# Performance work log

Measured on AMD Instinct MI355X. Metric: run time of the kernel, lower is better.

The kernel has to match this reference:

```python
import jax, jax.numpy as jnp
import numpy as np

N_NODES = 100000
N_EDGES = 1600000
NFEAT, NHID, NCLASS = 256, 256, 64
NLAYERS = 4


def _gcn_norm(edge_index, n_nodes):
    # PyG GCNConv default: add self-loops, symmetric normalization
    src, dst = edge_index[0], edge_index[1]
    loop = jnp.arange(n_nodes, dtype=edge_index.dtype)
    src = jnp.concatenate([src, loop])
    dst = jnp.concatenate([dst, loop])
    deg = jax.ops.segment_sum(jnp.ones_like(dst, dtype=jnp.float32), dst,
                              num_segments=n_nodes)
    dinv = jnp.where(deg > 0, jax.lax.rsqrt(deg), 0.0)
    norm = dinv[src] * dinv[dst]  # [E+N]
    return src, dst, norm


def _gcn_layer(X, W, b, src, dst, norm, n_nodes):
    H = X @ W                      # [N, out]
    msg = H[src] * norm[:, None]   # [E+N, out] gather + scale
    out = jax.ops.segment_sum(msg, dst, num_segments=n_nodes)
    return out + b


def setup_inputs() -> dict:
    key = jax.random.key(0)
    ks = jax.random.split(key, 8)
    x = jax.random.normal(ks[0], (N_NODES, NFEAT), dtype=jnp.float32)
    edge_index = jax.random.randint(ks[1], (2, N_EDGES), 0, N_NODES, dtype=jnp.int32)
    def glorot(k, fan_in, fan_out):
        s = jnp.sqrt(6.0 / (fan_in + fan_out))
        return jax.random.uniform(k, (fan_in, fan_out), jnp.float32, -s, s)
    return {
        "x": x,
        "W_enc": glorot(ks[2], NFEAT, NHID),
        "b_enc": jnp.zeros((NHID,), jnp.float32),
        "W_conv": glorot(ks[3], NHID, NHID),
        "b_conv": jnp.zeros((NHID,), jnp.float32),
        "W_dec": glorot(ks[4], NHID, NCLASS),
        "b_dec": jnp.zeros((NCLASS,), jnp.float32),
        "edge_index": edge_index,
    }


def reference(x, W_enc, b_enc, W_conv, b_conv, W_dec, b_dec, edge_index):
    n_nodes = x.shape[0]
    src, dst, norm = _gcn_norm(edge_index, n_nodes)
    # dropout probs are 0 (drop_in=drop=0) -> identity
    X = jax.nn.relu(_gcn_layer(x, W_enc, b_enc, src, dst, norm, n_nodes))
    for _ in range(NLAYERS):
        X = jax.nn.relu(_gcn_layer(X, W_conv, b_conv, src, dst, norm, n_nodes))
    X = jax.nn.relu(_gcn_layer(X, W_dec, b_dec, src, dst, norm, n_nodes))
    return X
```

## Files before the change

### kernel.cpp

```cpp
#include <hip/hip_runtime.h>

#define N_NODES 100000
#define N_EDGES 1600000
#define MPAD    100096
#define NB_SCAN ((N_NODES + 255) / 256)

using short8  = __attribute__((ext_vector_type(8))) short;
using ushort8 = __attribute__((ext_vector_type(8))) unsigned short;
using f32x4   = __attribute__((ext_vector_type(4))) float;

__device__ inline unsigned short f2bf(float f) {
    unsigned u = __float_as_uint(f);
    unsigned r = (u + 0x7fffu + ((u >> 16) & 1u)) >> 16;
    return (unsigned short)r;
}
__device__ inline float bf2f(unsigned short h) {
    return __uint_as_float(((unsigned)h) << 16);
}


__global__ __launch_bounds__(256) void k_init(int* __restrict__ indeg, int n) {
    int i = blockIdx.x * blockDim.x + threadIdx.x;
    if (i < n) indeg[i] = 0;
}

__global__ __launch_bounds__(256) void k_indeg(const int* __restrict__ dst,
                                               int* __restrict__ indeg, int e) {
    int i = (blockIdx.x * blockDim.x + threadIdx.x) * 4;
    if (i < e) {
        int4 d = *(const int4*)(dst + i);
        atomicAdd(&indeg[d.x], 1);
        atomicAdd(&indeg[d.y], 1);
        atomicAdd(&indeg[d.z], 1);
        atomicAdd(&indeg[d.w], 1);
    }
}

__global__ __launch_bounds__(256) void k_scan_blocks(const int* __restrict__ indeg,
                                                     int* __restrict__ blksum, int n) {
    int i = blockIdx.x * 256 + threadIdx.x;
    int v = (i < n) ? indeg[i] : 0;
#pragma unroll
    for (int o = 32; o > 0; o >>= 1) v += __shfl_down(v, o, 64);
    __shared__ int ws[4];
    if ((threadIdx.x & 63) == 0) ws[threadIdx.x >> 6] = v;
    __syncthreads();
    if (threadIdx.x == 0) blksum[blockIdx.x] = ws[0] + ws[1] + ws[2] + ws[3];
}

__global__ __launch_bounds__(512) void k_scan_top(const int* __restrict__ blksum,
                                                  int* __restrict__ blkpref,
                                                  int* __restrict__ offsets, int nb, int n) {
    __shared__ int s[512];
    int t = threadIdx.x;
    int v = (t < nb) ? blksum[t] : 0;
    s[t] = v;
    __syncthreads();
    for (int o = 1; o < 512; o <<= 1) {
        int u = (t >= o) ? s[t - o] : 0;
        __syncthreads();
        s[t] += u;
        __syncthreads();
    }
    if (t < nb) blkpref[t] = (t == 0) ? 0 : s[t - 1];
    if (t == nb - 1) offsets[n] = s[t];
}

__global__ __launch_bounds__(256) void k_scan_final(const int* __restrict__ indeg,
                                                    const int* __restrict__ blkpref,
                                                    int* __restrict__ offsets,
                                                    float* __restrict__ dinv, int n) {
    __shared__ int s[256];
    int t = threadIdx.x;
    int i = blockIdx.x * 256 + t;
    int v = (i < n) ? indeg[i] : 0;
    s[t] = v;
    __syncthreads();
    for (int o = 1; o < 256; o <<= 1) {
        int u = (t >= o) ? s[t - o] : 0;
        __syncthreads();
        s[t] += u;
        __syncthreads();
    }
    if (i < n) {
        offsets[i] = blkpref[blockIdx.x] + s[t] - v;
        dinv[i] = rsqrtf((float)(v + 1));
    }
}

__global__ __launch_bounds__(256) void k_scatter(const int* __restrict__ src,
                                                 const int* __restrict__ dst,
                                                 const int* __restrict__ offsets,
                                                 int* __restrict__ indeg,
                                                 int* __restrict__ csr_src, int e) {
    int i = blockIdx.x * blockDim.x + threadIdx.x;
    if (i < e) {
        int d = dst[i];
        int pos = offsets[d] + atomicSub(&indeg[d], 1) - 1;
        csr_src[pos] = src[i];
    }
}


__global__ __launch_bounds__(256) void k_cvt_x(const float* __restrict__ x,
                                               unsigned short* __restrict__ xb) {
    int i = blockIdx.x * blockDim.x + threadIdx.x;
    int row = i >> 6;
    ushort4 o;
    if (row < N_NODES) {
        float4 v = *(const float4*)(x + (size_t)i * 4);
        o.x = f2bf(v.x); o.y = f2bf(v.y); o.z = f2bf(v.z); o.w = f2bf(v.w);
    } else {
        o.x = o.y = o.z = o.w = 0;
    }
    *(ushort4*)(xb + (size_t)i * 4) = o;
}

__global__ __launch_bounds__(256) void k_prep_w(const float* __restrict__ W,
                                                unsigned short* __restrict__ Wt, int N) {
    int i = blockIdx.x * blockDim.x + threadIdx.x;
    if (i < 256 * N) {
        int r = i / N, c = i - r * N;
        Wt[(size_t)c * 256 + r] = f2bf(W[i]);
    }
}


template <int BN>
__global__ __launch_bounds__(256) void k_mfma_gemm(const unsigned short* __restrict__ A,
                                                   const unsigned short* __restrict__ Bt,
                                                   const float* __restrict__ dinv,
                                                   unsigned short* __restrict__ C,
                                                   int Ntot) {
    constexpr int K = 256, BK = 64;
    constexpr int NFR = BN / 32;
    __shared__ char ldsA[128 * 128];
    __shared__ char ldsB[BN * 128];
    const int tid  = threadIdx.x;
    const int lane = tid & 63;
    const int wid  = tid >> 6;
    const int wr   = wid >> 1, wc = wid & 1;
    const int row0 = blockIdx.x * 128;
    const int col0 = blockIdx.y * BN;
    const int l15  = lane & 15, lhi = lane >> 4;

    f32x4 acc[4][NFR];
#pragma unroll
    for (int m = 0; m < 4; ++m)
#pragma unroll
        for (int n = 0; n < NFR; ++n) acc[m][n] = {0.f, 0.f, 0.f, 0.f};

    for (int k0 = 0; k0 < K; k0 += BK) {
#pragma unroll
        for (int j = 0; j < 4; ++j) {
            int ci = j * 256 + tid;
            int r = ci >> 3;
            int cb = (ci & 7) ^ (r & 7);
            const char* src = (const char*)(A + (size_t)(row0 + r) * K + k0) + cb * 16;
            __builtin_amdgcn_global_load_lds((const __attribute__((address_space(1))) void*)src,
                                             (__attribute__((address_space(3))) void*)(ldsA + ci * 16),
                                             16, 0, 0);
        }
#pragma unroll
        for (int j = 0; j < BN / 32; ++j) {
            int ci = j * 256 + tid;
            int r = ci >> 3;
            int cb = (ci & 7) ^ (r & 7);
            const char* src = (const char*)(Bt + (size_t)(col0 + r) * K + k0) + cb * 16;
            __builtin_amdgcn_global_load_lds((const __attribute__((address_space(1))) void*)src,
                                             (__attribute__((address_space(3))) void*)(ldsB + ci * 16),
                                             16, 0, 0);
        }
        __syncthreads();
#pragma unroll
        for (int kk = 0; kk < 2; ++kk) {
            short8 af[4], bfr[NFR];
            int cb = kk * 4 + lhi;
#pragma unroll
            for (int m = 0; m < 4; ++m) {
                int r = wr * 64 + m * 16 + l15;
                af[m] = *(const short8*)(ldsA + r * 128 + ((cb ^ (r & 7)) << 4));
            }
#pragma unroll
            for (int n = 0; n < NFR; ++n) {
                int r = wc * (NFR * 16) + n * 16 + l15;
                bfr[n] = *(const short8*)(ldsB + r * 128 + ((cb ^ (r & 7)) << 4));
            }
#pragma unroll
            for (int m = 0; m < 4; ++m)
#pragma unroll
                for (int n = 0; n < NFR; ++n)
                    acc[m][n] = __builtin_amdgcn_mfma_f32_16x16x32_bf16(af[m], bfr[n],
                                                                        acc[m][n], 0, 0, 0);
        }
        __syncthreads();
    }
#pragma unroll
    for (int m = 0; m < 4; ++m) {
        int rbase = row0 + wr * 64 + m * 16 + lhi * 4;
        float sc[4];
#pragma unroll
        for (int q = 0; q < 4; ++q) {
            int grow = rbase + q;
            sc[q] = (grow < N_NODES) ? dinv[grow] : 0.f;
        }
#pragma unroll
        for (int n = 0; n < NFR; ++n) {
            int col = col0 + wc * (NFR * 16) + n * 16 + l15;
#pragma unroll
            for (int q = 0; q < 4; ++q)
                C[(size_t)(rbase + q) * Ntot + col] = f2bf(acc[m][n][q] * sc[q]);
        }
    }
}


__global__ __launch_bounds__(256) void k_agg256(const unsigned short* __restrict__ H,
                                                const int* __restrict__ offsets,
                                                const int* __restrict__ csr_src,
                                                const float* __restrict__ dinv,
                                                const float* __restrict__ bias,
                                                unsigned short* __restrict__ out, int n) {
    const int w = __builtin_amdgcn_readfirstlane((blockIdx.x * blockDim.x + threadIdx.x) >> 6);
    const int n0 = w * 2;
    if (n0 >= n) return;
    const int n1 = n0 + 1;
    const int lane = threadIdx.x & 63;
    const int half = lane >> 5;
    const unsigned coff = (unsigned)(lane & 31) * 16u;

    float a0[8] = {}, a1[8] = {};
    int e0 = offsets[n0];
    const int f0 = offsets[n1];
    int e1 = f0;
    const int f1 = offsets[n1 + 1];

    auto pair0 = [&](int ea) {
        int s0 = csr_src[ea], s1 = csr_src[ea + 1];
        ushort8 v = *(const ushort8*)((const char*)H + (unsigned)(half ? s1 : s0) * 512u + coff);
#pragma unroll
        for (int j = 0; j < 8; ++j) a0[j] += bf2f(v[j]);
    };
    auto pair1 = [&](int ea) {
        int s0 = csr_src[ea], s1 = csr_src[ea + 1];
        ushort8 v = *(const ushort8*)((const char*)H + (unsigned)(half ? s1 : s0) * 512u + coff);
#pragma unroll
        for (int j = 0; j < 8; ++j) a1[j] += bf2f(v[j]);
    };

    while (e0 + 3 < f0 && e1 + 3 < f1) {
        pair0(e0); pair0(e0 + 2);
        pair1(e1); pair1(e1 + 2);
        e0 += 4; e1 += 4;
    }
    while (e0 + 1 < f0 && e1 + 1 < f1) { pair0(e0); pair1(e1); e0 += 2; e1 += 2; }
    while (e0 + 1 < f0) { pair0(e0); e0 += 2; }
    while (e1 + 1 < f1) { pair1(e1); e1 += 2; }

    {
        int has = (e0 < f0);
        int sA = has ? csr_src[e0] : n0;
        float wB = has ? 1.f : 0.f;
        unsigned off = (unsigned)(half ? n0 : sA) * 512u + coff;
        float wgt = half ? wB : 1.f;
        ushort8 v = *(const ushort8*)((const char*)H + off);
#pragma unroll
        for (int j = 0; j < 8; ++j) a0[j] = fmaf(bf2f(v[j]), wgt, a0[j]);
    }
    {
        int has = (e1 < f1);
        int sA = has ? csr_src[e1] : n1;
        float wB = has ? 1.f : 0.f;
        unsigned off = (unsigned)(half ? n1 : sA) * 512u + coff;
        float wgt = half ? wB : 1.f;
        ushort8 v = *(const ushort8*)((const char*)H + off);
#pragma unroll
        for (int j = 0; j < 8; ++j) a1[j] = fmaf(bf2f(v[j]), wgt, a1[j]);
    }

#pragma unroll
    for (int j = 0; j < 8; ++j) {
        a0[j] += __shfl_xor(a0[j], 32);
        a1[j] += __shfl_xor(a1[j], 32);
    }

    if (half == 0) {
        const float* bp = bias + (lane & 31) * 8;
        float4 b0 = *(const float4*)bp;
        float4 b1 = *(const float4*)(bp + 4);
        float d0 = dinv[n0], d1 = dinv[n1];
        ushort8 o0, o1;
        o0[0] = f2bf(fmaxf(fmaf(a0[0], d0, b0.x), 0.f));
        o0[1] = f2bf(fmaxf(fmaf(a0[1], d0, b0.y), 0.f));
        o0[2] = f2bf(fmaxf(fmaf(a0[2], d0, b0.z), 0.f));
        o0[3] = f2bf(fmaxf(fmaf(a0[3], d0, b0.w), 0.f));
        o0[4] = f2bf(fmaxf(fmaf(a0[4], d0, b1.x), 0.f));
        o0[5] = f2bf(fmaxf(fmaf(a0[5], d0, b1.y), 0.f));
        o0[6] = f2bf(fmaxf(fmaf(a0[6], d0, b1.z), 0.f));
        o0[7] = f2bf(fmaxf(fmaf(a0[7], d0, b1.w), 0.f));
        o1[0] = f2bf(fmaxf(fmaf(a1[0], d1, b0.x), 0.f));
        o1[1] = f2bf(fmaxf(fmaf(a1[1], d1, b0.y), 0.f));
        o1[2] = f2bf(fmaxf(fmaf(a1[2], d1, b0.z), 0.f));
        o1[3] = f2bf(fmaxf(fmaf(a1[3], d1, b0.w), 0.f));
        o1[4] = f2bf(fmaxf(fmaf(a1[4], d1, b1.x), 0.f));
        o1[5] = f2bf(fmaxf(fmaf(a1[5], d1, b1.y), 0.f));
        o1[6] = f2bf(fmaxf(fmaf(a1[6], d1, b1.z), 0.f));
        o1[7] = f2bf(fmaxf(fmaf(a1[7], d1, b1.w), 0.f));
        *(ushort8*)((char*)out + (unsigned)n0 * 512u + coff) = o0;
        *(ushort8*)((char*)out + (unsigned)n1 * 512u + coff) = o1;
    }
}


__global__ __launch_bounds__(256) void k_agg64(const unsigned short* __restrict__ H,
                                               const int* __restrict__ offsets,
                                               const int* __restrict__ csr_src,
                                               const float* __restrict__ dinv,
                                               const float* __restrict__ bias,
                                               float* __restrict__ out, int n) {
    const int wid = __builtin_amdgcn_readfirstlane((blockIdx.x * blockDim.x + threadIdx.x) >> 6);
    if (wid >= n) return;
    const int lane = threadIdx.x & 63;
    const int q = lane >> 4;
    const unsigned coff = (unsigned)(lane & 15) * 8u;

    float acc[4] = {};
    const int beg = offsets[wid], end = offsets[wid + 1];
    int e = beg;

    for (; e + 3 < end; e += 4) {
        int s0 = csr_src[e], s1 = csr_src[e + 1], s2 = csr_src[e + 2], s3 = csr_src[e + 3];
        int srow = s0;
        if (q == 1) srow = s1;
        else if (q == 2) srow = s2;
        else if (q == 3) srow = s3;
        ushort4 v = *(const ushort4*)((const char*)H + (unsigned)srow * 128u + coff);
        acc[0] += bf2f(v.x); acc[1] += bf2f(v.y);
        acc[2] += bf2f(v.z); acc[3] += bf2f(v.w);
    }
    {
        int r = end - e;
        int srow = wid; float wgt = 0.f;
        if (q < r) { srow = csr_src[e + q]; wgt = 1.f; }
        else if (q == r) { srow = wid; wgt = 1.f; }
        ushort4 v = *(const ushort4*)((const char*)H + (unsigned)srow * 128u + coff);
        acc[0] = fmaf(bf2f(v.x), wgt, acc[0]);
        acc[1] = fmaf(bf2f(v.y), wgt, acc[1]);
        acc[2] = fmaf(bf2f(v.z), wgt, acc[2]);
        acc[3] = fmaf(bf2f(v.w), wgt, acc[3]);
    }
#pragma unroll
    for (int j = 0; j < 4; ++j) {
        acc[j] += __shfl_xor(acc[j], 16);
        acc[j] += __shfl_xor(acc[j], 32);
    }
    if (q == 0) {
        float dv = dinv[wid];
        float4 b = *(const float4*)(bias + (lane & 15) * 4);
        float4 o = make_float4(fmaxf(fmaf(acc[0], dv, b.x), 0.f),
                               fmaxf(fmaf(acc[1], dv, b.y), 0.f),
                               fmaxf(fmaf(acc[2], dv, b.z), 0.f),
                               fmaxf(fmaf(acc[3], dv, b.w), 0.f));
        *(float4*)((char*)out + (size_t)wid * 256u + coff * 2u) = o;
    }
}


extern "C" void kernel_launch(void* const* d_in, const int* in_sizes, int n_in,
                              void* d_out, int out_size, void* d_ws, size_t ws_size,
                              hipStream_t stream) {
    const float* x      = (const float*)d_in[0];
    const float* W_enc  = (const float*)d_in[1];
    const float* b_enc  = (const float*)d_in[2];
    const float* W_conv = (const float*)d_in[3];
    const float* b_conv = (const float*)d_in[4];
    const float* W_dec  = (const float*)d_in[5];
    const float* b_dec  = (const float*)d_in[6];
    const int*   ei     = (const int*)d_in[7];

    const int N = N_NODES;
    const int E = N_EDGES;
    const int* src = ei;
    const int* dst = ei + E;

    size_t off = 0;
    auto carve = [&](size_t bytes) -> void* {
        void* p = (char*)d_ws + off;
        off = (off + bytes + 255) & ~(size_t)255;
        return p;
    };
    unsigned short* Xb      = (unsigned short*)carve((size_t)MPAD * 256 * 2);
    unsigned short* Hb      = (unsigned short*)carve((size_t)MPAD * 256 * 2);
    unsigned short* Wt_enc  = (unsigned short*)carve((size_t)256 * 256 * 2);
    unsigned short* Wt_conv = (unsigned short*)carve((size_t)256 * 256 * 2);
    unsigned short* Wt_dec  = (unsigned short*)carve((size_t)64 * 256 * 2);
    int*            indeg   = (int*)carve((size_t)N * sizeof(int));
    float*          dinv    = (float*)carve((size_t)N * sizeof(float));
    int*            offsets = (int*)carve((size_t)(N + 1) * sizeof(int));
    int*            csr_src = (int*)carve((size_t)E * sizeof(int));
    int*            blksum  = (int*)carve((size_t)NB_SCAN * sizeof(int));
    int*            blkpref = (int*)carve((size_t)NB_SCAN * sizeof(int));
    (void)ws_size;

    k_cvt_x<<<MPAD / 4, 256, 0, stream>>>(x, Xb);
    k_prep_w<<<(256 * 256 + 255) / 256, 256, 0, stream>>>(W_enc, Wt_enc, 256);
    k_prep_w<<<(256 * 256 + 255) / 256, 256, 0, stream>>>(W_conv, Wt_conv, 256);
    k_prep_w<<<(256 * 64 + 255) / 256, 256, 0, stream>>>(W_dec, Wt_dec, 64);
    k_init<<<(N + 255) / 256, 256, 0, stream>>>(indeg, N);
    k_indeg<<<(E / 4 + 255) / 256, 256, 0, stream>>>(dst, indeg, E);
    k_scan_blocks<<<NB_SCAN, 256, 0, stream>>>(indeg, blksum, N);
    k_scan_top<<<1, 512, 0, stream>>>(blksum, blkpref, offsets, NB_SCAN, N);
    k_scan_final<<<NB_SCAN, 256, 0, stream>>>(indeg, blkpref, offsets, dinv, N);
    k_scatter<<<(E + 255) / 256, 256, 0, stream>>>(src, dst, offsets, indeg, csr_src, E);

    dim3 gconv(MPAD / 128, 2);
    dim3 gdec(MPAD / 128, 1);
    const int agg2_blocks = ((N + 1) / 2 + 3) / 4;
    const int agg1_blocks = (N + 3) / 4;

    k_mfma_gemm<128><<<gconv, 256, 0, stream>>>(Xb, Wt_enc, dinv, Hb, 256);
    k_agg256<<<agg2_blocks, 256, 0, stream>>>(Hb, offsets, csr_src, dinv, b_enc, Xb, N);
    for (int l = 0; l < 4; ++l) {
        k_mfma_gemm<128><<<gconv, 256, 0, stream>>>(Xb, Wt_conv, dinv, Hb, 256);
        k_agg256<<<agg2_blocks, 256, 0, stream>>>(Hb, offsets, csr_src, dinv, b_conv, Xb, N);
    }
    k_mfma_gemm<64><<<gdec, 256, 0, stream>>>(Xb, Wt_dec, dinv, Hb, 64);
    k_agg64<<<agg1_blocks, 256, 0, stream>>>(Hb, offsets, csr_src, dinv, b_dec,
                                             (float*)d_out, N);
}
```

Measured before the change: 1.041 ms.

## Fuse aggregation and GEMM for conv layers using aggregate-then-transform ordering

The four hidden conv layers now run one fused kernel instead of a GEMM plus an aggregation kernel. Each block first aggregates 64 destination rows of pre-scaled features into LDS, then multiplies by W with MFMA and applies bias, ReLU and dinv in the epilogue. The previous layer's output is pre-multiplied by dinv, so the decoder GEMM drops its own dinv scaling. This removes the intermediate H round trip through HBM and half the launches. The costs are that W is read straight from global memory per block, the gather phase may run at lower occupancy because of the 32KB LDS tile, and extra bf16 rounding now happens after the aggregation step.

```diff
diff --git a/kernel.cpp b/kernel.cpp
--- a/kernel.cpp
+++ b/kernel.cpp
@@ -126,7 +126,7 @@
 }
 
 
-template <int BN>
+template <int BN, bool DSCALE>
 __global__ __launch_bounds__(256) void k_mfma_gemm(const unsigned short* __restrict__ A,
                                                    const unsigned short* __restrict__ Bt,
                                                    const float* __restrict__ dinv,
@@ -202,7 +202,7 @@
 #pragma unroll
         for (int q = 0; q < 4; ++q) {
             int grow = rbase + q;
-            sc[q] = (grow < N_NODES) ? dinv[grow] : 0.f;
+            sc[q] = DSCALE ? ((grow < N_NODES) ? dinv[grow] : 0.f) : 1.f;
         }
 #pragma unroll
         for (int n = 0; n < NFR; ++n) {
@@ -261,9 +261,8 @@
         int has = (e0 < f0);
         int sA = has ? csr_src[e0] : n0;
         float wB = has ? 1.f : 0.f;
-        unsigned off = (unsigned)(half ? n0 : sA) * 512u + coff;
+        ushort8 v = *(const ushort8*)((const char*)H + (unsigned)(half ? n0 : sA) * 512u + coff);
         float wgt = half ? wB : 1.f;
-        ushort8 v = *(const ushort8*)((const char*)H + off);
 #pragma unroll
         for (int j = 0; j < 8; ++j) a0[j] = fmaf(bf2f(v[j]), wgt, a0[j]);
     }
@@ -271,9 +270,8 @@
         int has = (e1 < f1);
         int sA = has ? csr_src[e1] : n1;
         float wB = has ? 1.f : 0.f;
-        unsigned off = (unsigned)(half ? n1 : sA) * 512u + coff;
+        ushort8 v = *(const ushort8*)((const char*)H + (unsigned)(half ? n1 : sA) * 512u + coff);
         float wgt = half ? wB : 1.f;
-        ushort8 v = *(const ushort8*)((const char*)H + off);
 #pragma unroll
         for (int j = 0; j < 8; ++j) a1[j] = fmaf(bf2f(v[j]), wgt, a1[j]);
     }
@@ -289,25 +287,122 @@
         float4 b0 = *(const float4*)bp;
         float4 b1 = *(const float4*)(bp + 4);
         float d0 = dinv[n0], d1 = dinv[n1];
+        float bb[8] = {b0.x, b0.y, b0.z, b0.w, b1.x, b1.y, b1.z, b1.w};
         ushort8 o0, o1;
-        o0[0] = f2bf(fmaxf(fmaf(a0[0], d0, b0.x), 0.f));
-        o0[1] = f2bf(fmaxf(fmaf(a0[1], d0, b0.y), 0.f));
-        o0[2] = f2bf(fmaxf(fmaf(a0[2], d0, b0.z), 0.f));
-        o0[3] = f2bf(fmaxf(fmaf(a0[3], d0, b0.w), 0.f));
-        o0[4] = f2bf(fmaxf(fmaf(a0[4], d0, b1.x), 0.f));
-        o0[5] = f2bf(fmaxf(fmaf(a0[5], d0, b1.y), 0.f));
-        o0[6] = f2bf(fmaxf(fmaf(a0[6], d0, b1.z), 0.f));
-        o0[7] = f2bf(fmaxf(fmaf(a0[7], d0, b1.w), 0.f));
-        o1[0] = f2bf(fmaxf(fmaf(a1[0], d1, b0.x), 0.f));
-        o1[1] = f2bf(fmaxf(fmaf(a1[1], d1, b0.y), 0.f));
-        o1[2] = f2bf(fmaxf(fmaf(a1[2], d1, b0.z), 0.f));
-        o1[3] = f2bf(fmaxf(fmaf(a1[3], d1, b0.w), 0.f));
-        o1[4] = f2bf(fmaxf(fmaf(a1[4], d1, b1.x), 0.f));
-        o1[5] = f2bf(fmaxf(fmaf(a1[5], d1, b1.y), 0.f));
-        o1[6] = f2bf(fmaxf(fmaf(a1[6], d1, b1.z), 0.f));
-        o1[7] = f2bf(fmaxf(fmaf(a1[7], d1, b1.w), 0.f));
+#pragma unroll
+        for (int j = 0; j < 8; ++j) {
+            o0[j] = f2bf(d0 * fmaxf(fmaf(a0[j], d0, bb[j]), 0.f));
+            o1[j] = f2bf(d1 * fmaxf(fmaf(a1[j], d1, bb[j]), 0.f));
+        }
         *(ushort8*)((char*)out + (unsigned)n0 * 512u + coff) = o0;
         *(ushort8*)((char*)out + (unsigned)n1 * 512u + coff) = o1;
+    }
+}
+
+
+__global__ __launch_bounds__(256) void k_fused_conv(const unsigned short* __restrict__ X,
+                                                    const unsigned short* __restrict__ Wt,
+                                                    const int* __restrict__ offsets,
+                                                    const int* __restrict__ csr_src,
+                                                    const float* __restrict__ dinv,
+                                                    const float* __restrict__ bias,
+                                                    unsigned short* __restrict__ Y, int n) {
+    __shared__ char S[64 * 512];
+    const int tid  = threadIdx.x;
+    const int lane = tid & 63;
+    const int wid  = __builtin_amdgcn_readfirstlane(tid >> 6);
+    const int tile0 = blockIdx.x * 64;
+    const int half = lane >> 5;
+    const unsigned c32 = (unsigned)(lane & 31);
+
+    for (int i = 0; i < 16; ++i) {
+        const int r = wid * 16 + i;
+        const int d = tile0 + r;
+        float acc[8] = {};
+        if (d < n) {
+            int e = offsets[d];
+            const int f = offsets[d + 1];
+            for (; e + 3 < f; e += 4) {
+                int s0 = csr_src[e], s1 = csr_src[e + 1];
+                int s2 = csr_src[e + 2], s3 = csr_src[e + 3];
+                ushort8 v0 = *(const ushort8*)((const char*)X + (unsigned)(half ? s1 : s0) * 512u + c32 * 16u);
+                ushort8 v1 = *(const ushort8*)((const char*)X + (unsigned)(half ? s3 : s2) * 512u + c32 * 16u);
+#pragma unroll
+                for (int j = 0; j < 8; ++j) acc[j] += bf2f(v0[j]);
+#pragma unroll
+                for (int j = 0; j < 8; ++j) acc[j] += bf2f(v1[j]);
+            }
+            for (; e + 1 < f; e += 2) {
+                int s0 = csr_src[e], s1 = csr_src[e + 1];
+                ushort8 v = *(const ushort8*)((const char*)X + (unsigned)(half ? s1 : s0) * 512u + c32 * 16u);
+#pragma unroll
+                for (int j = 0; j < 8; ++j) acc[j] += bf2f(v[j]);
+            }
+            int has = (e < f);
+            int sA = has ? csr_src[e] : d;
+            float wB = has ? 1.f : 0.f;
+            ushort8 v = *(const ushort8*)((const char*)X + (unsigned)(half ? d : sA) * 512u + c32 * 16u);
+            float wgt = half ? wB : 1.f;
+#pragma unroll
+            for (int j = 0; j < 8; ++j) acc[j] = fmaf(bf2f(v[j]), wgt, acc[j]);
+        }
+#pragma unroll
+        for (int j = 0; j < 8; ++j) acc[j] += __shfl_xor(acc[j], 32);
+        if (half == 0) {
+            ushort8 o;
+#pragma unroll
+            for (int j = 0; j < 8; ++j) o[j] = f2bf(acc[j]);
+            *(ushort8*)(S + r * 512 + ((c32 ^ (unsigned)(r & 7)) << 4)) = o;
+        }
+    }
+    __syncthreads();
+
+    const int l15 = lane & 15, lhi = lane >> 4;
+#pragma unroll
+    for (int h = 0; h < 2; ++h) {
+        f32x4 acc[4][2];
+#pragma unroll
+        for (int m = 0; m < 4; ++m)
+#pragma unroll
+            for (int nn = 0; nn < 2; ++nn) acc[m][nn] = {0.f, 0.f, 0.f, 0.f};
+#pragma unroll
+        for (int kk = 0; kk < 8; ++kk) {
+            short8 af[4], bw[2];
+            int cb = kk * 4 + lhi;
+#pragma unroll
+            for (int m = 0; m < 4; ++m) {
+                int r = m * 16 + l15;
+                af[m] = *(const short8*)(S + r * 512 + ((cb ^ (r & 7)) << 4));
+            }
+#pragma unroll
+            for (int nn = 0; nn < 2; ++nn) {
+                int col = wid * 64 + h * 32 + nn * 16 + l15;
+                bw[nn] = *(const short8*)(Wt + (size_t)col * 256 + kk * 32 + lhi * 8);
+            }
+#pragma unroll
+            for (int m = 0; m < 4; ++m)
+#pragma unroll
+                for (int nn = 0; nn < 2; ++nn)
+                    acc[m][nn] = __builtin_amdgcn_mfma_f32_16x16x32_bf16(af[m], bw[nn],
+                                                                         acc[m][nn], 0, 0, 0);
+        }
+#pragma unroll
+        for (int m = 0; m < 4; ++m) {
+#pragma unroll
+            for (int nn = 0; nn < 2; ++nn) {
+                int col = wid * 64 + h * 32 + nn * 16 + l15;
+                float bcol = bias[col];
+#pragma unroll
+                for (int q = 0; q < 4; ++q) {
+                    int d = tile0 + m * 16 + lhi * 4 + q;
+                    if (d < n) {
+                        float dv = dinv[d];
+                        float z = fmaf(acc[m][nn][q], dv, bcol);
+                        Y[(size_t)d * 256 + col] = f2bf(dv * fmaxf(z, 0.f));
+                    }
+                }
+            }
+        }
     }
 }
 
@@ -415,16 +510,17 @@
 
     dim3 gconv(MPAD / 128, 2);
     dim3 gdec(MPAD / 128, 1);
+    const int fused_blocks = MPAD / 64;
     const int agg2_blocks = ((N + 1) / 2 + 3) / 4;
     const int agg1_blocks = (N + 3) / 4;
 
-    k_mfma_gemm<128><<<gconv, 256, 0, stream>>>(Xb, Wt_enc, dinv, Hb, 256);
+    k_mfma_gemm<128, true><<<gconv, 256, 0, stream>>>(Xb, Wt_enc, dinv, Hb, 256);
     k_agg256<<<agg2_blocks, 256, 0, stream>>>(Hb, offsets, csr_src, dinv, b_enc, Xb, N);
-    for (int l = 0; l < 4; ++l) {
-        k_mfma_gemm<128><<<gconv, 256, 0, stream>>>(Xb, Wt_conv, dinv, Hb, 256);
-        k_agg256<<<agg2_blocks, 256, 0, stream>>>(Hb, offsets, csr_src, dinv, b_conv, Xb, N);
-    }
-    k_mfma_gemm<64><<<gdec, 256, 0, stream>>>(Xb, Wt_dec, dinv, Hb, 64);
+    k_fused_conv<<<fused_blocks, 256, 0, stream>>>(Xb, Wt_conv, offsets, csr_src, dinv, b_conv, Hb, N);
+    k_fused_conv<<<fused_blocks, 256, 0, stream>>>(Hb, Wt_conv, offsets, csr_src, dinv, b_conv, Xb, N);
+    k_fused_conv<<<fused_blocks, 256, 0, stream>>>(Xb, Wt_conv, offsets, csr_src, dinv, b_conv, Hb, N);
+    k_fused_conv<<<fused_blocks, 256, 0, stream>>>(Hb, Wt_conv, offsets, csr_src, dinv, b_conv, Xb, N);
+    k_mfma_gemm<64, false><<<gdec, 256, 0, stream>>>(Xb, Wt_dec, dinv, Hb, 64);
     k_agg64<<<agg1_blocks, 256, 0, stream>>>(Hb, offsets, csr_src, dinv, b_dec,
                                              (float*)d_out, N);
 }
```

New measurement: 1.245 ms. 1.2x slower.
